# Kernel tuning notes

Measured on AMD Instinct MI355X. Metric: run time of the kernel, lower is better.

Reference implementation:

```python
import jax, jax.numpy as jnp
import numpy as np

T = 4096          # num tokens
HID = 2048        # hidden_size
HQ = 32           # num q heads
HKV = 8           # num kv heads
G = HQ // HKV     # GQA group size
D = 128           # head_dim (q/k)
DV = 96           # v_head_dim
W = 512           # sliding window (= query block size)
THETA = 1e6
Q_SIZE, K_SIZE, V_SIZE = HQ * D, HKV * D, HKV * DV


def setup_inputs() -> dict:
    key = jax.random.key(0)
    k1, k2, k3, k4 = jax.random.split(key, 4)
    positions = jnp.arange(T, dtype=jnp.int32)
    hidden_states = jax.random.normal(k1, (T, HID), dtype=jnp.float32)
    qkv_w = jax.random.normal(k2, (Q_SIZE + K_SIZE + V_SIZE, HID), dtype=jnp.float32) * (HID ** -0.5)
    o_w = jax.random.normal(k3, (HID, HQ * DV), dtype=jnp.float32) * ((HQ * DV) ** -0.5)
    sink_bias = jax.random.normal(k4, (HQ,), dtype=jnp.float32)
    return {"positions": positions, "hidden_states": hidden_states,
            "qkv_w": qkv_w, "o_w": o_w, "sink_bias": sink_bias}


def _rope(x, positions):
    # neox-style rotate-half RoPE on full head_dim (partial_rotary_factor=1.0)
    half = D // 2
    inv_freq = 1.0 / (THETA ** (jnp.arange(0, half, dtype=jnp.float32) / half))
    ang = positions.astype(jnp.float32)[:, None] * inv_freq[None, :]   # [T, D/2]
    cos = jnp.cos(ang)[:, None, :]
    sin = jnp.sin(ang)[:, None, :]
    x1, x2 = x[..., :half], x[..., half:]
    return jnp.concatenate([x1 * cos - x2 * sin, x2 * cos + x1 * sin], axis=-1)


def _swa_with_sink(q, k, v, sink_bias):
    # q: [T, HKV, G, D], k: [T, HKV, D], v: [T, HKV, DV]
    nb = T // W
    scale = D ** -0.5
    qb = q.reshape(nb, W, HKV, G, D)
    # per query block i, keys/values from global span [(i-1)*W, (i+1)*W)
    k_pad = jnp.pad(k, ((W, 0), (0, 0), (0, 0)))
    v_pad = jnp.pad(v, ((W, 0), (0, 0), (0, 0)))
    idx = jnp.arange(nb)[:, None] * W + jnp.arange(2 * W)[None, :]     # [nb, 2W]
    k_ext = k_pad[idx]                                                 # [nb, 2W, HKV, D]
    v_ext = v_pad[idx]                                                 # [nb, 2W, HKV, DV]
    # mask: rel = t - j in [0, W); exclude left-pad keys (key_pos < 0)
    r = jnp.arange(W)[:, None]
    c = jnp.arange(2 * W)[None, :]
    rel = W + r - c                                                    # [W, 2W]
    key_pos = (jnp.arange(nb)[:, None, None] - 1) * W + c[None]        # [nb, W(1), 2W]
    mask = (rel >= 0) & (rel < W) & (key_pos >= 0)                     # [nb, W, 2W]
    scores = jnp.einsum('nrkgd,nckd->nkgrc', qb, k_ext) * scale        # [nb,HKV,G,W,2W]
    scores = jnp.where(mask[:, None, None, :, :], scores, -jnp.inf)
    sink = jnp.broadcast_to(sink_bias.reshape(HKV, G)[None, :, :, None, None],
                            (nb, HKV, G, W, 1))
    logits = jnp.concatenate([scores, sink], axis=-1)                  # [...,2W+1]
    p = jax.nn.softmax(logits, axis=-1)[..., :-1]                      # drop sink column
    out = jnp.einsum('nkgrc,nckd->nrkgd', p, v_ext)                    # [nb,W,HKV,G,DV]
    return out.reshape(T, HQ * DV)


def reference(positions, hidden_states, qkv_w, o_w, sink_bias):
    qkv = hidden_states @ qkv_w.T                                      # [T, Q+K+V]
    q, k, v = jnp.split(qkv, [Q_SIZE, Q_SIZE + K_SIZE], axis=-1)
    q = q.reshape(T, HQ, D)
    k = k.reshape(T, HKV, D)
    v = v.reshape(T, HKV, DV)
    q = _rope(q, positions).reshape(T, HKV, G, D)
    k = _rope(k, positions)
    attn = _swa_with_sink(q, k, v, sink_bias)                          # [T, HQ*DV]
    return attn @ o_w.T                                                # [T, HID]
```

## Files before the change

### kernel.cpp

```cpp
#include <hip/hip_runtime.h>
#include <hip/hip_bf16.h>
#include <stdint.h>

#define T_SEQ 4096
#define HIDDEN 2048
#define NQH 32
#define NKVH 8
#define DH 128
#define DVH 96
#define WWIN 512
#define QKVN 5888
#define KOFF 4096
#define VOFF 5120
#define ATTN 3072
#define QSCALE 0.08838834764831845f

typedef uint16_t u16;
typedef uint32_t u32;
typedef __bf16 bfrag8 __attribute__((ext_vector_type(8)));
typedef float f32x4v __attribute__((ext_vector_type(4)));
typedef float f32x16 __attribute__((ext_vector_type(16)));

__device__ __forceinline__ u16 f2bf(float x) {
  u32 u = __float_as_uint(x);
  return (u16)((u + 0x7fffu + ((u >> 16) & 1u)) >> 16);
}
__device__ __forceinline__ float bf2f(u16 v) { return __uint_as_float(((u32)v) << 16); }

__device__ __forceinline__ void gload16(const u16* src, char* ldst) {
  __builtin_amdgcn_global_load_lds((const __attribute__((address_space(1))) u32*)src,
                                   (__attribute__((address_space(3))) u32*)ldst, 16, 0, 0);
}

__global__ void cvt_kernel(const float* __restrict__ in, u16* __restrict__ out, int n4) {
  int i = blockIdx.x * blockDim.x + threadIdx.x;
  int st = gridDim.x * blockDim.x;
  for (; i < n4; i += st) {
    float4 v = ((const float4*)in)[i];
    ushort4 o;
    o.x = f2bf(v.x); o.y = f2bf(v.y); o.z = f2bf(v.z); o.w = f2bf(v.w);
    ((ushort4*)out)[i] = o;
  }
}

template<int OUT_F32>
__global__ __launch_bounds__(512, 2) void gemm_v3(const u16* __restrict__ A,
                                                  const u16* __restrict__ B,
                                                  void* __restrict__ Cp,
                                                  int M, int N, int K, int nbm) {
  extern __shared__ char lds[];
  const int tid = threadIdx.x;
  const int w = tid >> 6, lane = tid & 63;
  const int wr = w >> 1, wc = w & 1;
  const int r5 = lane & 31, kg = lane >> 5;

  const int nwg = gridDim.x;
  int bid = (int)blockIdx.x;
  if ((nwg & 7) == 0) bid = (bid & 7) * (nwg >> 3) + (bid >> 3);
  const int bm = (bid % nbm) * 256;
  const int bn = (bid / nbm) * 128;
  const int NT = K >> 6;

  f32x16 acc[2][2];
#pragma unroll
  for (int mb = 0; mb < 2; mb++)
#pragma unroll
    for (int nb = 0; nb < 2; nb++)
#pragma unroll
      for (int i = 0; i < 16; i++) acc[mb][nb][i] = 0.f;

  const int q = r5 * 128 + ((kg ^ (r5 & 7)) << 4);

  auto stageA = [&](int t) {
    char* dst = lds + (t % 3) * 49152;
    const u16* Abase = A + (size_t)bm * K + ((size_t)t << 6);
#pragma unroll
    for (int i = 0; i < 4; i++) {
      int D = (w * 4 + i) * 1024 + lane * 16;
      int row = D >> 7;
      int kb = (D ^ ((row & 7) << 4)) & 127;
      gload16(Abase + (size_t)row * K + (kb >> 1), dst + D);
    }
  };
  auto stageB = [&](int t) {
    char* dst = lds + (t % 3) * 49152 + 32768;
    const u16* Bbase = B + (size_t)bn * K + ((size_t)t << 6);
#pragma unroll
    for (int i = 0; i < 2; i++) {
      int D = (w * 2 + i) * 1024 + lane * 16;
      int row = D >> 7;
      int kb = (D ^ ((row & 7) << 4)) & 127;
      gload16(Bbase + (size_t)row * K + (kb >> 1), dst + D);
    }
  };

  stageA(0); stageB(0);

  for (int t = 0; t < NT; ++t) {
    const char* Ab = lds + (t % 3) * 49152 + wr * 8192;
    const char* Bb = lds + (t % 3) * 49152 + 32768 + wc * 8192;
    if (t + 1 < NT) {
      stageA(t + 1);
      stageB(t + 1);
      asm volatile("s_waitcnt vmcnt(6)");
    } else {
      asm volatile("s_waitcnt vmcnt(0)");
    }
    asm volatile("s_barrier" ::: "memory");

    bfrag8 af[2][2], bf[2][2];
#pragma unroll
    for (int ks = 0; ks < 2; ks++) {
#pragma unroll
      for (int mb = 0; mb < 2; mb++)
        af[mb][ks] = *(const bfrag8*)(Ab + mb * 4096 + (q ^ (ks << 5)));
#pragma unroll
      for (int nb = 0; nb < 2; nb++)
        bf[nb][ks] = *(const bfrag8*)(Bb + nb * 4096 + (q ^ (ks << 5)));
    }
    __builtin_amdgcn_s_setprio(1);
#pragma unroll
    for (int ks = 0; ks < 2; ks++)
#pragma unroll
      for (int mb = 0; mb < 2; mb++)
#pragma unroll
        for (int nb = 0; nb < 2; nb++)
          acc[mb][nb] = __builtin_amdgcn_mfma_f32_32x32x16_bf16(af[mb][ks], bf[nb][ks], acc[mb][nb], 0, 0, 0);
    __builtin_amdgcn_s_setprio(0);

    bfrag8 af2[2][2], bf2[2][2];
#pragma unroll
    for (int ks = 0; ks < 2; ks++) {
#pragma unroll
      for (int mb = 0; mb < 2; mb++)
        af2[mb][ks] = *(const bfrag8*)(Ab + mb * 4096 + (q ^ ((ks + 2) << 5)));
#pragma unroll
      for (int nb = 0; nb < 2; nb++)
        bf2[nb][ks] = *(const bfrag8*)(Bb + nb * 4096 + (q ^ ((ks + 2) << 5)));
    }
    __builtin_amdgcn_s_setprio(1);
#pragma unroll
    for (int ks = 0; ks < 2; ks++)
#pragma unroll
      for (int mb = 0; mb < 2; mb++)
#pragma unroll
        for (int nb = 0; nb < 2; nb++)
          acc[mb][nb] = __builtin_amdgcn_mfma_f32_32x32x16_bf16(af2[mb][ks], bf2[nb][ks], acc[mb][nb], 0, 0, 0);
    __builtin_amdgcn_s_setprio(0);
  }

  const int rb0 = bm + wr * 64;
  const int cb0 = bn + wc * 64;
#pragma unroll
  for (int mb = 0; mb < 2; mb++)
#pragma unroll
    for (int nb = 0; nb < 2; nb++)
#pragma unroll
      for (int i = 0; i < 16; i++) {
        int rowl = (i & 3) + 8 * (i >> 2) + 4 * kg;
        size_t off = (size_t)(rb0 + mb * 32 + rowl) * N + cb0 + nb * 32 + r5;
        if (OUT_F32) ((float*)Cp)[off] = acc[mb][nb][i];
        else         ((u16*)Cp)[off] = f2bf(acc[mb][nb][i]);
      }
}

template<int OUT_F32>
__global__ __launch_bounds__(256) void gemm_nt(const u16* __restrict__ A,
                                               const u16* __restrict__ B,
                                               void* __restrict__ Cp,
                                               int M, int N, int K) {
  __shared__ u16 Asm[128 * 32];
  __shared__ u16 Bsm[128 * 32];
  const int tid = threadIdx.x;
  const int wv = tid >> 6, lane = tid & 63;
  const int bm = blockIdx.x * 128, bn = blockIdx.y * 128;
  const int wm = (wv >> 1) * 64, wn = (wv & 1) * 64;
  const int srow = lane >> 2;
  const int scol = (lane & 3) * 8;
  const int fr = lane & 15, fk = (lane >> 4) * 8;
  f32x4v acc[4][4];
#pragma unroll
  for (int i = 0; i < 4; i++)
#pragma unroll
    for (int j = 0; j < 4; j++) acc[i][j] = {0.f, 0.f, 0.f, 0.f};

  for (int kt = 0; kt < K; kt += 32) {
    __syncthreads();
#pragma unroll
    for (int c = 0; c < 2; c++) {
      const int ci = wv * 2 + c;
      const u16* ga = A + (size_t)(bm + ci * 16 + srow) * K + kt + scol;
      const u16* gb = B + (size_t)(bn + ci * 16 + srow) * K + kt + scol;
      gload16(ga, (char*)(Asm + ci * 512));
      gload16(gb, (char*)(Bsm + ci * 512));
    }
    __syncthreads();
    bfrag8 af[4], bf[4];
#pragma unroll
    for (int i = 0; i < 4; i++) af[i] = *(const bfrag8*)(Asm + (wm + i * 16 + fr) * 32 + fk);
#pragma unroll
    for (int j = 0; j < 4; j++) bf[j] = *(const bfrag8*)(Bsm + (wn + j * 16 + fr) * 32 + fk);
#pragma unroll
    for (int i = 0; i < 4; i++)
#pragma unroll
      for (int j = 0; j < 4; j++)
        acc[i][j] = __builtin_amdgcn_mfma_f32_16x16x32_bf16(af[i], bf[j], acc[i][j], 0, 0, 0);
  }
  const int orow = (lane >> 4) * 4, ocol = lane & 15;
#pragma unroll
  for (int i = 0; i < 4; i++)
#pragma unroll
    for (int j = 0; j < 4; j++) {
      size_t base = (size_t)(bm + wm + i * 16 + orow) * N + (size_t)(bn + wn + j * 16 + ocol);
#pragma unroll
      for (int r = 0; r < 4; r++) {
        if (OUT_F32) ((float*)Cp)[base + (size_t)r * N] = acc[i][j][r];
        else         ((u16*)Cp)[base + (size_t)r * N] = f2bf(acc[i][j][r]);
      }
    }
}

__global__ void rope_kernel(u16* __restrict__ qkv, const int* __restrict__ pos) {
  int gid = blockIdx.x * 256 + threadIdx.x;
  int d = gid & 63;
  int r = gid >> 6;
  int hh = r % 40;
  int t = r / 40;
  if (t >= T_SEQ) return;
  int off = (hh < 32) ? hh * 128 : KOFF + (hh - 32) * 128;
  u16* p = qkv + (size_t)t * QKVN + off + d;
  float x1 = bf2f(p[0]);
  float x2 = bf2f(p[64]);
  float inv_freq = exp2f(-(float)d * 0.3114307588956852f);
  float ang = (float)pos[t] * inv_freq;
  float c = cosf(ang), s = sinf(ang);
  float y1 = x1 * c - x2 * s;
  float y2 = x2 * c + x1 * s;
  if (hh < 32) { y1 *= QSCALE; y2 *= QSCALE; }
  p[0] = f2bf(y1);
  p[64] = f2bf(y2);
}

__global__ __launch_bounds__(256) void vt_kernel(const u16* __restrict__ qkv,
                                                 u16* __restrict__ vt) {
  __shared__ u16 tile[64][100];
  const int t0 = blockIdx.x * 64;
  const int hk = blockIdx.y;
  const int tid = threadIdx.x;
#pragma unroll
  for (int i = 0; i < 3; i++) {
    int idx = i * 256 + tid;
    int row = idx / 12, ch = idx % 12;
    const u16* g = qkv + (size_t)(t0 + row) * QKVN + VOFF + hk * DVH + ch * 8;
    uint2 a = *(const uint2*)g;
    uint2 b = *(const uint2*)(g + 4);
    *(uint2*)&tile[row][ch * 8] = a;
    *(uint2*)&tile[row][ch * 8 + 4] = b;
  }
  __syncthreads();
#pragma unroll
  for (int i = 0; i < 3; i++) {
    int idx = i * 256 + tid;
    int dv = idx >> 3, tc = (idx & 7) * 8;
    union { uint4 v4; u16 s[8]; } o;
#pragma unroll
    for (int j = 0; j < 8; j++) o.s[j] = tile[tc + j][dv];
    *(uint4*)(vt + (((size_t)(hk * 96 + dv)) << 12) + t0 + tc) = o.v4;
  }
}

__global__ __launch_bounds__(256, 2) void attn_mfma(const u16* __restrict__ qkv,
                                                    const u16* __restrict__ vt,
                                                    const float* __restrict__ sink_bias,
                                                    u16* __restrict__ attn_out) {
  extern __shared__ char smem[];

  const int tid = threadIdx.x;
  const int wv = tid >> 6;
  const int lane = tid & 63;
  const int g = lane >> 4;
  const int c = lane & 15;
  const int t0 = blockIdx.x * 32;
  const int hk = blockIdx.y;
  const int h = hk * 4 + wv;
  u16* pw = (u16*)(smem + 57344 + wv * 4096);

  bfrag8 qf[2][4];
#pragma unroll
  for (int m = 0; m < 2; m++)
#pragma unroll
    for (int kf = 0; kf < 4; kf++)
      qf[m][kf] = *(const bfrag8*)(qkv + (size_t)(t0 + m * 16 + c) * QKVN + h * DH + kf * 32 + g * 8);

  f32x4v acc_o[2][6];
#pragma unroll
  for (int m = 0; m < 2; m++)
#pragma unroll
    for (int n = 0; n < 6; n++) acc_o[m][n] = {0.f, 0.f, 0.f, 0.f};

  const float sb = sink_bias[h];
  float m_run[2][4], l_run[2][4];
#pragma unroll
  for (int m = 0; m < 2; m++)
#pragma unroll
    for (int r = 0; r < 4; r++) { m_run[m][r] = sb; l_run[m][r] = 1.0f; }

  int cb0 = t0 - (WWIN - 1);
  cb0 = (cb0 < 0) ? 0 : (cb0 & ~63);
  const int nc = (t0 + 32 - cb0 + 63) >> 6;

  auto stage = [&](int ci) {
    const int cb = cb0 + ci * 64;
    char* kd = smem + (ci & 1) * 16384;
    char* vd = smem + 32768 + (ci & 1) * 12288;
#pragma unroll
    for (int it = 0; it < 4; it++) {
      int dest = it * 4096 + tid * 16;
      int row = dest >> 8;
      int src = dest ^ ((row & 7) << 4);
      gload16(qkv + (size_t)(cb + row) * QKVN + KOFF + hk * DH + ((src & 255) >> 1), kd + dest);
    }
#pragma unroll
    for (int it = 0; it < 3; it++) {
      int dest = it * 4096 + tid * 16;
      int row = dest >> 7;
      int src = dest ^ ((row & 7) << 4);
      gload16(vt + (((size_t)(hk * 96 + row)) << 12) + cb + ((src & 127) >> 1), vd + dest);
    }
  };

  stage(0);
  if (nc > 1) stage(1);

  for (int ci = 0; ci < nc; ci++) {
    const int cb = cb0 + ci * 64;
    const char* k_lds = smem + (ci & 1) * 16384;
    const char* v_lds = smem + 32768 + (ci & 1) * 12288;
    if (ci + 1 < nc) asm volatile("s_waitcnt vmcnt(7)");
    else             asm volatile("s_waitcnt vmcnt(0)");
    asm volatile("s_barrier" ::: "memory");

    f32x4v s[2][4];
#pragma unroll
    for (int m = 0; m < 2; m++)
#pragma unroll
      for (int n = 0; n < 4; n++) s[m][n] = {0.f, 0.f, 0.f, 0.f};
#pragma unroll
    for (int kf = 0; kf < 4; kf++) {
      bfrag8 kb[4];
#pragma unroll
      for (int n = 0; n < 4; n++) {
        int key = n * 16 + c;
        int byt = ((key << 8) + (kf << 6) + (g << 4)) ^ ((key & 7) << 4);
        kb[n] = *(const bfrag8*)(k_lds + byt);
      }
#pragma unroll
      for (int m = 0; m < 2; m++)
#pragma unroll
        for (int n = 0; n < 4; n++)
          s[m][n] = __builtin_amdgcn_mfma_f32_16x16x32_bf16(qf[m][kf], kb[n], s[m][n], 0, 0, 0);
    }

    if ((cb + 63 > t0) || (cb + WWIN < t0 + 32)) {
#pragma unroll
      for (int m = 0; m < 2; m++)
#pragma unroll
        for (int n = 0; n < 4; n++)
#pragma unroll
          for (int r = 0; r < 4; r++) {
            int rel = (t0 + m * 16 + g * 4 + r) - (cb + n * 16 + c);
            if (!(rel >= 0 && rel < WWIN)) s[m][n][r] = -3.0e38f;
          }
    }

    float corr[2][4];
#pragma unroll
    for (int m = 0; m < 2; m++)
#pragma unroll
      for (int r = 0; r < 4; r++) {
        float v0 = fmaxf(fmaxf(s[m][0][r], s[m][1][r]), fmaxf(s[m][2][r], s[m][3][r]));
        v0 = fmaxf(v0, __shfl_xor(v0, 1));
        v0 = fmaxf(v0, __shfl_xor(v0, 2));
        v0 = fmaxf(v0, __shfl_xor(v0, 4));
        v0 = fmaxf(v0, __shfl_xor(v0, 8));
        float mn = fmaxf(m_run[m][r], v0);
        corr[m][r] = __expf(m_run[m][r] - mn);
        m_run[m][r] = mn;
        float p0 = __expf(s[m][0][r] - mn);
        float p1 = __expf(s[m][1][r] - mn);
        float p2 = __expf(s[m][2][r] - mn);
        float p3 = __expf(s[m][3][r] - mn);
        s[m][0][r] = p0; s[m][1][r] = p1; s[m][2][r] = p2; s[m][3][r] = p3;
        float rs = p0 + p1 + p2 + p3;
        rs += __shfl_xor(rs, 1);
        rs += __shfl_xor(rs, 2);
        rs += __shfl_xor(rs, 4);
        rs += __shfl_xor(rs, 8);
        l_run[m][r] = l_run[m][r] * corr[m][r] + rs;
      }
#pragma unroll
    for (int m = 0; m < 2; m++)
#pragma unroll
      for (int n = 0; n < 6; n++)
#pragma unroll
      for (int r = 0; r < 4; r++) acc_o[m][n][r] *= corr[m][r];

#pragma unroll
    for (int m = 0; m < 2; m++)
#pragma unroll
      for (int n = 0; n < 4; n++) {
        u32 lo = (u32)f2bf(s[m][n][0]) | ((u32)f2bf(s[m][n][1]) << 16);
        u32 hi = (u32)f2bf(s[m][n][2]) | ((u32)f2bf(s[m][n][3]) << 16);
        int byt = ((m * 2 + (n >> 1)) << 10) | (g << 3) | ((c & 3) << 5) |
                  (((c >> 2) & 1) << 9) | ((((n & 1) * 2) + (c >> 3)) << 7);
        uint2 u; u.x = lo; u.y = hi;
        *(uint2*)((char*)pw + byt) = u;
      }

#pragma unroll
    for (int ks = 0; ks < 2; ks++) {
      bfrag8 pa[2];
#pragma unroll
      for (int m = 0; m < 2; m++) {
        union { bfrag8 v; u16 s16[8]; } u;
#pragma unroll
        for (int j = 0; j < 4; j++) {
          int e = ((m * 2 + ks) << 9) + c + j * 16 + g * 64;
          u.s16[j] = pw[e];
          u.s16[4 + j] = pw[e + 256];
        }
        pa[m] = u.v;
      }
#pragma unroll
      for (int n = 0; n < 6; n++) {
        int dv = n * 16 + c;
        int byt = ((dv << 7) + (ks << 6) + (g << 4)) ^ ((dv & 7) << 4);
        bfrag8 vb = *(const bfrag8*)(v_lds + byt);
#pragma unroll
        for (int m = 0; m < 2; m++)
          acc_o[m][n] = __builtin_amdgcn_mfma_f32_16x16x32_bf16(pa[m], vb, acc_o[m][n], 0, 0, 0);
      }
    }

    asm volatile("s_barrier" ::: "memory");
    if (ci + 2 < nc) stage(ci + 2);
  }

#pragma unroll
  for (int m = 0; m < 2; m++) {
    float inv[4];
#pragma unroll
    for (int r = 0; r < 4; r++) inv[r] = 1.0f / l_run[m][r];
#pragma unroll
    for (int n = 0; n < 6; n++)
#pragma unroll
      for (int r = 0; r < 4; r++) {
        int tq = t0 + m * 16 + g * 4 + r;
        attn_out[(size_t)tq * ATTN + h * DVH + n * 16 + c] = f2bf(acc_o[m][n][r] * inv[r]);
      }
  }
}

extern "C" void kernel_launch(void* const* d_in, const int* in_sizes, int n_in,
                              void* d_out, int out_size, void* d_ws, size_t ws_size,
                              hipStream_t stream) {
  const int* positions = (const int*)d_in[0];
  const float* hidden = (const float*)d_in[1];
  const float* qkv_w = (const float*)d_in[2];
  const float* o_w = (const float*)d_in[3];
  const float* sink = (const float*)d_in[4];
  char* ws = (char*)d_ws;

  u16* hs_bf   = (u16*)(ws + 0);
  u16* w1_bf   = (u16*)(ws + 16777216);
  u16* attn_bf = (u16*)(ws + 0);
  u16* vt_buf  = (u16*)(ws + 25165824);
  u16* w2_bf   = (u16*)(ws + 40894464);
  u16* qkv_bf  = (u16*)(ws + 53477376);

  bool v3Ok =
    (hipFuncSetAttribute((const void*)&gemm_v3<0>,
                         hipFuncAttributeMaxDynamicSharedMemorySize, 147456) == hipSuccess) &&
    (hipFuncSetAttribute((const void*)&gemm_v3<1>,
                         hipFuncAttributeMaxDynamicSharedMemorySize, 147456) == hipSuccess);
  bool atOk = (hipFuncSetAttribute((const void*)&attn_mfma,
                 hipFuncAttributeMaxDynamicSharedMemorySize, 73728) == hipSuccess);
  (void)atOk;

  cvt_kernel<<<dim3(1024), dim3(256), 0, stream>>>(hidden, hs_bf, 8388608 / 4);
  cvt_kernel<<<dim3(1024), dim3(256), 0, stream>>>(qkv_w, w1_bf, 12058624 / 4);
  cvt_kernel<<<dim3(1024), dim3(256), 0, stream>>>(o_w, w2_bf, 6291456 / 4);

  if (v3Ok)
    gemm_v3<0><<<dim3(736), dim3(512), 147456, stream>>>(hs_bf, w1_bf, (void*)qkv_bf,
                                                         T_SEQ, QKVN, HIDDEN, 16);
  else
    gemm_nt<0><<<dim3(32, 46), dim3(256), 0, stream>>>(hs_bf, w1_bf, (void*)qkv_bf,
                                                       T_SEQ, QKVN, HIDDEN);

  rope_kernel<<<dim3(40960), dim3(256), 0, stream>>>(qkv_bf, positions);
  vt_kernel<<<dim3(T_SEQ / 64, NKVH), dim3(256), 0, stream>>>(qkv_bf, vt_buf);
  attn_mfma<<<dim3(T_SEQ / 32, NKVH), dim3(256), 73728, stream>>>(qkv_bf, vt_buf, sink, attn_bf);

  if (v3Ok)
    gemm_v3<1><<<dim3(256), dim3(512), 147456, stream>>>(attn_bf, w2_bf, d_out,
                                                         T_SEQ, HIDDEN, ATTN, 16);
  else
    gemm_nt<1><<<dim3(32, 16), dim3(256), 0, stream>>>(attn_bf, w2_bf, d_out,
                                                       T_SEQ, HIDDEN, ATTN);
}
```

Before: 313.5 us.

## Double attention query tile, vectorize RoPE, fuse fp32→bf16 conversions into one launch

The attention kernel now processes 64 queries per block instead of 32, split into two 32-row halves per KV chunk. Each staged K/V chunk is reused across twice as many queries, cutting redundant global loads and the block count. The output rescale is skipped when no running max grew, RoPE handles 8 elements per thread with 16-byte loads, and the three conversion kernels are merged into one launch. The larger query tile raises register pressure (qf, acc_o and softmax state double) and halves grid parallelism for attention.

```diff
diff --git a/kernel.cpp b/kernel.cpp
--- a/kernel.cpp
+++ b/kernel.cpp
@@ -32,14 +32,24 @@
                                    (__attribute__((address_space(3))) u32*)ldst, 16, 0, 0);
 }
 
-__global__ void cvt_kernel(const float* __restrict__ in, u16* __restrict__ out, int n4) {
+__global__ void cvt3_kernel(const float* __restrict__ i1, const float* __restrict__ i2,
+                            const float* __restrict__ i3,
+                            u16* __restrict__ o1, u16* __restrict__ o2, u16* __restrict__ o3,
+                            int n1, int n2, int n3) {
   int i = blockIdx.x * blockDim.x + threadIdx.x;
   int st = gridDim.x * blockDim.x;
-  for (; i < n4; i += st) {
-    float4 v = ((const float4*)in)[i];
+  int total = n1 + n2 + n3;
+  for (; i < total; i += st) {
+    const float4* src;
+    ushort4* dst;
+    int j;
+    if (i < n1) { src = (const float4*)i1; dst = (ushort4*)o1; j = i; }
+    else if (i < n1 + n2) { src = (const float4*)i2; dst = (ushort4*)o2; j = i - n1; }
+    else { src = (const float4*)i3; dst = (ushort4*)o3; j = i - n1 - n2; }
+    float4 v = src[j];
     ushort4 o;
     o.x = f2bf(v.x); o.y = f2bf(v.y); o.z = f2bf(v.z); o.w = f2bf(v.w);
-    ((ushort4*)out)[i] = o;
+    dst[j] = o;
   }
 }
 
@@ -222,23 +232,33 @@
 
 __global__ void rope_kernel(u16* __restrict__ qkv, const int* __restrict__ pos) {
   int gid = blockIdx.x * 256 + threadIdx.x;
-  int d = gid & 63;
-  int r = gid >> 6;
+  int dc = gid & 7;
+  int r = gid >> 3;
   int hh = r % 40;
   int t = r / 40;
   if (t >= T_SEQ) return;
   int off = (hh < 32) ? hh * 128 : KOFF + (hh - 32) * 128;
-  u16* p = qkv + (size_t)t * QKVN + off + d;
-  float x1 = bf2f(p[0]);
-  float x2 = bf2f(p[64]);
-  float inv_freq = exp2f(-(float)d * 0.3114307588956852f);
-  float ang = (float)pos[t] * inv_freq;
-  float c = cosf(ang), s = sinf(ang);
-  float y1 = x1 * c - x2 * s;
-  float y2 = x2 * c + x1 * s;
-  if (hh < 32) { y1 *= QSCALE; y2 *= QSCALE; }
-  p[0] = f2bf(y1);
-  p[64] = f2bf(y2);
+  u16* p = qkv + (size_t)t * QKVN + off + dc * 8;
+  uint4 a = *(const uint4*)p;
+  uint4 b = *(const uint4*)(p + 64);
+  const u32* aw = (const u32*)&a;
+  const u32* bw = (const u32*)&b;
+  float pt = (float)pos[t];
+  float sc = (hh < 32) ? QSCALE : 1.0f;
+  union { uint4 v; u16 s[8]; } ra, rb;
+#pragma unroll
+  for (int j = 0; j < 8; j++) {
+    int d = dc * 8 + j;
+    float inv_freq = exp2f(-(float)d * 0.3114307588956852f);
+    float ang = pt * inv_freq;
+    float cs = cosf(ang), sn = sinf(ang);
+    float x1 = bf2f((u16)(aw[j >> 1] >> ((j & 1) * 16)));
+    float x2 = bf2f((u16)(bw[j >> 1] >> ((j & 1) * 16)));
+    ra.s[j] = f2bf((x1 * cs - x2 * sn) * sc);
+    rb.s[j] = f2bf((x2 * cs + x1 * sn) * sc);
+  }
+  *(uint4*)p = ra.v;
+  *(uint4*)(p + 64) = rb.v;
 }
 
 __global__ __launch_bounds__(256) void vt_kernel(const u16* __restrict__ qkv,
@@ -280,34 +300,34 @@
   const int lane = tid & 63;
   const int g = lane >> 4;
   const int c = lane & 15;
-  const int t0 = blockIdx.x * 32;
+  const int t0 = blockIdx.x * 64;
   const int hk = blockIdx.y;
   const int h = hk * 4 + wv;
   u16* pw = (u16*)(smem + 57344 + wv * 4096);
 
-  bfrag8 qf[2][4];
-#pragma unroll
-  for (int m = 0; m < 2; m++)
+  bfrag8 qf[4][4];
+#pragma unroll
+  for (int m = 0; m < 4; m++)
 #pragma unroll
     for (int kf = 0; kf < 4; kf++)
       qf[m][kf] = *(const bfrag8*)(qkv + (size_t)(t0 + m * 16 + c) * QKVN + h * DH + kf * 32 + g * 8);
 
-  f32x4v acc_o[2][6];
-#pragma unroll
-  for (int m = 0; m < 2; m++)
+  f32x4v acc_o[4][6];
+#pragma unroll
+  for (int m = 0; m < 4; m++)
 #pragma unroll
     for (int n = 0; n < 6; n++) acc_o[m][n] = {0.f, 0.f, 0.f, 0.f};
 
   const float sb = sink_bias[h];
-  float m_run[2][4], l_run[2][4];
-#pragma unroll
-  for (int m = 0; m < 2; m++)
+  float m_run[4][4], l_run[4][4];
+#pragma unroll
+  for (int m = 0; m < 4; m++)
 #pragma unroll
     for (int r = 0; r < 4; r++) { m_run[m][r] = sb; l_run[m][r] = 1.0f; }
 
   int cb0 = t0 - (WWIN - 1);
   cb0 = (cb0 < 0) ? 0 : (cb0 & ~63);
-  const int nc = (t0 + 32 - cb0 + 63) >> 6;
+  const int nc = ((t0 - cb0) >> 6) + 1;
 
   auto stage = [&](int ci) {
     const int cb = cb0 + ci * 64;
@@ -340,105 +360,116 @@
     else             asm volatile("s_waitcnt vmcnt(0)");
     asm volatile("s_barrier" ::: "memory");
 
-    f32x4v s[2][4];
-#pragma unroll
-    for (int m = 0; m < 2; m++)
-#pragma unroll
-      for (int n = 0; n < 4; n++) s[m][n] = {0.f, 0.f, 0.f, 0.f};
-#pragma unroll
-    for (int kf = 0; kf < 4; kf++) {
-      bfrag8 kb[4];
-#pragma unroll
-      for (int n = 0; n < 4; n++) {
-        int key = n * 16 + c;
-        int byt = ((key << 8) + (kf << 6) + (g << 4)) ^ ((key & 7) << 4);
-        kb[n] = *(const bfrag8*)(k_lds + byt);
-      }
-#pragma unroll
-      for (int m = 0; m < 2; m++)
-#pragma unroll
-        for (int n = 0; n < 4; n++)
-          s[m][n] = __builtin_amdgcn_mfma_f32_16x16x32_bf16(qf[m][kf], kb[n], s[m][n], 0, 0, 0);
-    }
-
-    if ((cb + 63 > t0) || (cb + WWIN < t0 + 32)) {
-#pragma unroll
-      for (int m = 0; m < 2; m++)
-#pragma unroll
-        for (int n = 0; n < 4; n++)
-#pragma unroll
-          for (int r = 0; r < 4; r++) {
-            int rel = (t0 + m * 16 + g * 4 + r) - (cb + n * 16 + c);
-            if (!(rel >= 0 && rel < WWIN)) s[m][n][r] = -3.0e38f;
+    const bool edge = (cb + 63 > t0) || (cb + WWIN < t0 + 64);
+
+#pragma unroll
+    for (int mh = 0; mh < 2; mh++) {
+      f32x4v s[2][4];
+#pragma unroll
+      for (int ml = 0; ml < 2; ml++)
+#pragma unroll
+        for (int n = 0; n < 4; n++) s[ml][n] = {0.f, 0.f, 0.f, 0.f};
+#pragma unroll
+      for (int kf = 0; kf < 4; kf++) {
+        bfrag8 kb[4];
+#pragma unroll
+        for (int n = 0; n < 4; n++) {
+          int key = n * 16 + c;
+          int byt = ((key << 8) + (kf << 6) + (g << 4)) ^ ((key & 7) << 4);
+          kb[n] = *(const bfrag8*)(k_lds + byt);
+        }
+#pragma unroll
+        for (int ml = 0; ml < 2; ml++)
+#pragma unroll
+          for (int n = 0; n < 4; n++)
+            s[ml][n] = __builtin_amdgcn_mfma_f32_16x16x32_bf16(qf[mh * 2 + ml][kf], kb[n], s[ml][n], 0, 0, 0);
+      }
+
+      if (edge) {
+#pragma unroll
+        for (int ml = 0; ml < 2; ml++)
+#pragma unroll
+          for (int n = 0; n < 4; n++)
+#pragma unroll
+            for (int r = 0; r < 4; r++) {
+              int rel = (t0 + (mh * 2 + ml) * 16 + g * 4 + r) - (cb + n * 16 + c);
+              if (!(rel >= 0 && rel < WWIN)) s[ml][n][r] = -3.0e38f;
+            }
+      }
+
+      float corr[2][4];
+      bool grew = false;
+#pragma unroll
+      for (int ml = 0; ml < 2; ml++)
+#pragma unroll
+        for (int r = 0; r < 4; r++) {
+          const int M = mh * 2 + ml;
+          float v0 = fmaxf(fmaxf(s[ml][0][r], s[ml][1][r]), fmaxf(s[ml][2][r], s[ml][3][r]));
+          v0 = fmaxf(v0, __shfl_xor(v0, 1));
+          v0 = fmaxf(v0, __shfl_xor(v0, 2));
+          v0 = fmaxf(v0, __shfl_xor(v0, 4));
+          v0 = fmaxf(v0, __shfl_xor(v0, 8));
+          float mo = m_run[M][r];
+          float mn = fmaxf(mo, v0);
+          corr[ml][r] = __expf(mo - mn);
+          grew |= (mn > mo);
+          m_run[M][r] = mn;
+          float p0 = __expf(s[ml][0][r] - mn);
+          float p1 = __expf(s[ml][1][r] - mn);
+          float p2 = __expf(s[ml][2][r] - mn);
+          float p3 = __expf(s[ml][3][r] - mn);
+          s[ml][0][r] = p0; s[ml][1][r] = p1; s[ml][2][r] = p2; s[ml][3][r] = p3;
+          float rs = p0 + p1 + p2 + p3;
+          rs += __shfl_xor(rs, 1);
+          rs += __shfl_xor(rs, 2);
+          rs += __shfl_xor(rs, 4);
+          rs += __shfl_xor(rs, 8);
+          l_run[M][r] = l_run[M][r] * corr[ml][r] + rs;
+        }
+      if (__any(grew)) {
+#pragma unroll
+        for (int ml = 0; ml < 2; ml++)
+#pragma unroll
+          for (int n = 0; n < 6; n++)
+#pragma unroll
+            for (int r = 0; r < 4; r++) acc_o[mh * 2 + ml][n][r] *= corr[ml][r];
+      }
+
+#pragma unroll
+      for (int ml = 0; ml < 2; ml++)
+#pragma unroll
+        for (int n = 0; n < 4; n++) {
+          u32 lo = (u32)f2bf(s[ml][n][0]) | ((u32)f2bf(s[ml][n][1]) << 16);
+          u32 hi = (u32)f2bf(s[ml][n][2]) | ((u32)f2bf(s[ml][n][3]) << 16);
+          int byt = ((ml * 2 + (n >> 1)) << 10) | (g << 3) | ((c & 3) << 5) |
+                    (((c >> 2) & 1) << 9) | ((((n & 1) * 2) + (c >> 3)) << 7);
+          uint2 u; u.x = lo; u.y = hi;
+          *(uint2*)((char*)pw + byt) = u;
+        }
+
+#pragma unroll
+      for (int ks = 0; ks < 2; ks++) {
+        bfrag8 pa[2];
+#pragma unroll
+        for (int ml = 0; ml < 2; ml++) {
+          union { bfrag8 v; u16 s16[8]; } u;
+#pragma unroll
+          for (int j = 0; j < 4; j++) {
+            int e = ((ml * 2 + ks) << 9) + c + j * 16 + g * 64;
+            u.s16[j] = pw[e];
+            u.s16[4 + j] = pw[e + 256];
           }
-    }
-
-    float corr[2][4];
-#pragma unroll
-    for (int m = 0; m < 2; m++)
-#pragma unroll
-      for (int r = 0; r < 4; r++) {
-        float v0 = fmaxf(fmaxf(s[m][0][r], s[m][1][r]), fmaxf(s[m][2][r], s[m][3][r]));
-        v0 = fmaxf(v0, __shfl_xor(v0, 1));
-        v0 = fmaxf(v0, __shfl_xor(v0, 2));
-        v0 = fmaxf(v0, __shfl_xor(v0, 4));
-        v0 = fmaxf(v0, __shfl_xor(v0, 8));
-        float mn = fmaxf(m_run[m][r], v0);
-        corr[m][r] = __expf(m_run[m][r] - mn);
-        m_run[m][r] = mn;
-        float p0 = __expf(s[m][0][r] - mn);
-        float p1 = __expf(s[m][1][r] - mn);
-        float p2 = __expf(s[m][2][r] - mn);
-        float p3 = __expf(s[m][3][r] - mn);
-        s[m][0][r] = p0; s[m][1][r] = p1; s[m][2][r] = p2; s[m][3][r] = p3;
-        float rs = p0 + p1 + p2 + p3;
-        rs += __shfl_xor(rs, 1);
-        rs += __shfl_xor(rs, 2);
-        rs += __shfl_xor(rs, 4);
-        rs += __shfl_xor(rs, 8);
-        l_run[m][r] = l_run[m][r] * corr[m][r] + rs;
-      }
-#pragma unroll
-    for (int m = 0; m < 2; m++)
-#pragma unroll
-      for (int n = 0; n < 6; n++)
-#pragma unroll
-      for (int r = 0; r < 4; r++) acc_o[m][n][r] *= corr[m][r];
-
-#pragma unroll
-    for (int m = 0; m < 2; m++)
-#pragma unroll
-      for (int n = 0; n < 4; n++) {
-        u32 lo = (u32)f2bf(s[m][n][0]) | ((u32)f2bf(s[m][n][1]) << 16);
-        u32 hi = (u32)f2bf(s[m][n][2]) | ((u32)f2bf(s[m][n][3]) << 16);
-        int byt = ((m * 2 + (n >> 1)) << 10) | (g << 3) | ((c & 3) << 5) |
-                  (((c >> 2) & 1) << 9) | ((((n & 1) * 2) + (c >> 3)) << 7);
-        uint2 u; u.x = lo; u.y = hi;
-        *(uint2*)((char*)pw + byt) = u;
-      }
-
-#pragma unroll
-    for (int ks = 0; ks < 2; ks++) {
-      bfrag8 pa[2];
-#pragma unroll
-      for (int m = 0; m < 2; m++) {
-        union { bfrag8 v; u16 s16[8]; } u;
-#pragma unroll
-        for (int j = 0; j < 4; j++) {
-          int e = ((m * 2 + ks) << 9) + c + j * 16 + g * 64;
-          u.s16[j] = pw[e];
-          u.s16[4 + j] = pw[e + 256];
+          pa[ml] = u.v;
         }
-        pa[m] = u.v;
-      }
-#pragma unroll
-      for (int n = 0; n < 6; n++) {
-        int dv = n * 16 + c;
-        int byt = ((dv << 7) + (ks << 6) + (g << 4)) ^ ((dv & 7) << 4);
-        bfrag8 vb = *(const bfrag8*)(v_lds + byt);
-#pragma unroll
-        for (int m = 0; m < 2; m++)
-          acc_o[m][n] = __builtin_amdgcn_mfma_f32_16x16x32_bf16(pa[m], vb, acc_o[m][n], 0, 0, 0);
+#pragma unroll
+        for (int n = 0; n < 6; n++) {
+          int dv = n * 16 + c;
+          int byt = ((dv << 7) + (ks << 6) + (g << 4)) ^ ((dv & 7) << 4);
+          bfrag8 vb = *(const bfrag8*)(v_lds + byt);
+#pragma unroll
+          for (int ml = 0; ml < 2; ml++)
+            acc_o[mh * 2 + ml][n] = __builtin_amdgcn_mfma_f32_16x16x32_bf16(pa[ml], vb, acc_o[mh * 2 + ml][n], 0, 0, 0);
+        }
       }
     }
 
@@ -447,7 +478,7 @@
   }
 
 #pragma unroll
-  for (int m = 0; m < 2; m++) {
+  for (int m = 0; m < 4; m++) {
     float inv[4];
 #pragma unroll
     for (int r = 0; r < 4; r++) inv[r] = 1.0f / l_run[m][r];
@@ -483,13 +514,12 @@
                          hipFuncAttributeMaxDynamicSharedMemorySize, 147456) == hipSuccess) &&
     (hipFuncSetAttribute((const void*)&gemm_v3<1>,
                          hipFuncAttributeMaxDynamicSharedMemorySize, 147456) == hipSuccess);
-  bool atOk = (hipFuncSetAttribute((const void*)&attn_mfma,
-                 hipFuncAttributeMaxDynamicSharedMemorySize, 73728) == hipSuccess);
-  (void)atOk;
-
-  cvt_kernel<<<dim3(1024), dim3(256), 0, stream>>>(hidden, hs_bf, 8388608 / 4);
-  cvt_kernel<<<dim3(1024), dim3(256), 0, stream>>>(qkv_w, w1_bf, 12058624 / 4);
-  cvt_kernel<<<dim3(1024), dim3(256), 0, stream>>>(o_w, w2_bf, 6291456 / 4);
+  (void)hipFuncSetAttribute((const void*)&attn_mfma,
+                            hipFuncAttributeMaxDynamicSharedMemorySize, 73728);
+
+  cvt3_kernel<<<dim3(2048), dim3(256), 0, stream>>>(hidden, qkv_w, o_w,
+                                                    hs_bf, w1_bf, w2_bf,
+                                                    2097152, 3014656, 1572864);
 
   if (v3Ok)
     gemm_v3<0><<<dim3(736), dim3(512), 147456, stream>>>(hs_bf, w1_bf, (void*)qkv_bf,
@@ -498,9 +528,9 @@
     gemm_nt<0><<<dim3(32, 46), dim3(256), 0, stream>>>(hs_bf, w1_bf, (void*)qkv_bf,
                                                        T_SEQ, QKVN, HIDDEN);
 
-  rope_kernel<<<dim3(40960), dim3(256), 0, stream>>>(qkv_bf, positions);
+  rope_kernel<<<dim3(5120), dim3(256), 0, stream>>>(qkv_bf, positions);
   vt_kernel<<<dim3(T_SEQ / 64, NKVH), dim3(256), 0, stream>>>(qkv_bf, vt_buf);
-  attn_mfma<<<dim3(T_SEQ / 32, NKVH), dim3(256), 73728, stream>>>(qkv_bf, vt_buf, sink, attn_bf);
+  attn_mfma<<<dim3(T_SEQ / 64, NKVH), dim3(256), 73728, stream>>>(qkv_bf, vt_buf, sink, attn_bf);
 
   if (v3Ok)
     gemm_v3<1><<<dim3(256), dim3(512), 147456, stream>>>(attn_bf, w2_bf, d_out,
```

After: 385.4 us. 1.23x slower.

## Fuse weight conversions, vectorize RoPE, skip unneeded accumulator rescale

Applied to the files above, without the earlier changes.

Merges the three fp32-to-bf16 conversion launches into one kernel over the concatenated ranges, which saves launch overhead and tail effects. Changes RoPE so each thread handles 8 contiguous elements with 128-bit loads and stores instead of scalar 16-bit accesses, which also cuts the grid size by 8x. In the attention loop, the output accumulator rescale is skipped when no row's running max grew in the wave. This adds a wave vote and branch in exchange for fewer multiplies.

```diff
diff --git a/kernel.cpp b/kernel.cpp
--- a/kernel.cpp
+++ b/kernel.cpp
@@ -32,14 +32,24 @@
                                    (__attribute__((address_space(3))) u32*)ldst, 16, 0, 0);
 }
 
-__global__ void cvt_kernel(const float* __restrict__ in, u16* __restrict__ out, int n4) {
+__global__ void cvt3_kernel(const float* __restrict__ i1, const float* __restrict__ i2,
+                            const float* __restrict__ i3,
+                            u16* __restrict__ o1, u16* __restrict__ o2, u16* __restrict__ o3,
+                            int n1, int n2, int n3) {
   int i = blockIdx.x * blockDim.x + threadIdx.x;
   int st = gridDim.x * blockDim.x;
-  for (; i < n4; i += st) {
-    float4 v = ((const float4*)in)[i];
+  int total = n1 + n2 + n3;
+  for (; i < total; i += st) {
+    const float4* src;
+    ushort4* dst;
+    int j;
+    if (i < n1) { src = (const float4*)i1; dst = (ushort4*)o1; j = i; }
+    else if (i < n1 + n2) { src = (const float4*)i2; dst = (ushort4*)o2; j = i - n1; }
+    else { src = (const float4*)i3; dst = (ushort4*)o3; j = i - n1 - n2; }
+    float4 v = src[j];
     ushort4 o;
     o.x = f2bf(v.x); o.y = f2bf(v.y); o.z = f2bf(v.z); o.w = f2bf(v.w);
-    ((ushort4*)out)[i] = o;
+    dst[j] = o;
   }
 }
 
@@ -222,23 +232,33 @@
 
 __global__ void rope_kernel(u16* __restrict__ qkv, const int* __restrict__ pos) {
   int gid = blockIdx.x * 256 + threadIdx.x;
-  int d = gid & 63;
-  int r = gid >> 6;
+  int dc = gid & 7;
+  int r = gid >> 3;
   int hh = r % 40;
   int t = r / 40;
   if (t >= T_SEQ) return;
   int off = (hh < 32) ? hh * 128 : KOFF + (hh - 32) * 128;
-  u16* p = qkv + (size_t)t * QKVN + off + d;
-  float x1 = bf2f(p[0]);
-  float x2 = bf2f(p[64]);
-  float inv_freq = exp2f(-(float)d * 0.3114307588956852f);
-  float ang = (float)pos[t] * inv_freq;
-  float c = cosf(ang), s = sinf(ang);
-  float y1 = x1 * c - x2 * s;
-  float y2 = x2 * c + x1 * s;
-  if (hh < 32) { y1 *= QSCALE; y2 *= QSCALE; }
-  p[0] = f2bf(y1);
-  p[64] = f2bf(y2);
+  u16* p = qkv + (size_t)t * QKVN + off + dc * 8;
+  uint4 a = *(const uint4*)p;
+  uint4 b = *(const uint4*)(p + 64);
+  const u32* aw = (const u32*)&a;
+  const u32* bw = (const u32*)&b;
+  float pt = (float)pos[t];
+  float sc = (hh < 32) ? QSCALE : 1.0f;
+  union { uint4 v; u16 s[8]; } ra, rb;
+#pragma unroll
+  for (int j = 0; j < 8; j++) {
+    int d = dc * 8 + j;
+    float inv_freq = exp2f(-(float)d * 0.3114307588956852f);
+    float ang = pt * inv_freq;
+    float cs = cosf(ang), sn = sinf(ang);
+    float x1 = bf2f((u16)(aw[j >> 1] >> ((j & 1) * 16)));
+    float x2 = bf2f((u16)(bw[j >> 1] >> ((j & 1) * 16)));
+    ra.s[j] = f2bf((x1 * cs - x2 * sn) * sc);
+    rb.s[j] = f2bf((x2 * cs + x1 * sn) * sc);
+  }
+  *(uint4*)p = ra.v;
+  *(uint4*)(p + 64) = rb.v;
 }
 
 __global__ __launch_bounds__(256) void vt_kernel(const u16* __restrict__ qkv,
@@ -374,6 +394,7 @@
     }
 
     float corr[2][4];
+    bool grew = false;
 #pragma unroll
     for (int m = 0; m < 2; m++)
 #pragma unroll
@@ -383,8 +404,10 @@
         v0 = fmaxf(v0, __shfl_xor(v0, 2));
         v0 = fmaxf(v0, __shfl_xor(v0, 4));
         v0 = fmaxf(v0, __shfl_xor(v0, 8));
-        float mn = fmaxf(m_run[m][r], v0);
-        corr[m][r] = __expf(m_run[m][r] - mn);
+        float mo = m_run[m][r];
+        float mn = fmaxf(mo, v0);
+        corr[m][r] = __expf(mo - mn);
+        grew |= (mn > mo);
         m_run[m][r] = mn;
         float p0 = __expf(s[m][0][r] - mn);
         float p1 = __expf(s[m][1][r] - mn);
@@ -398,12 +421,14 @@
         rs += __shfl_xor(rs, 8);
         l_run[m][r] = l_run[m][r] * corr[m][r] + rs;
       }
-#pragma unroll
-    for (int m = 0; m < 2; m++)
-#pragma unroll
-      for (int n = 0; n < 6; n++)
-#pragma unroll
-      for (int r = 0; r < 4; r++) acc_o[m][n][r] *= corr[m][r];
+    if (__any(grew)) {
+#pragma unroll
+      for (int m = 0; m < 2; m++)
+#pragma unroll
+        for (int n = 0; n < 6; n++)
+#pragma unroll
+        for (int r = 0; r < 4; r++) acc_o[m][n][r] *= corr[m][r];
+    }
 
 #pragma unroll
     for (int m = 0; m < 2; m++)
@@ -483,13 +508,12 @@
                          hipFuncAttributeMaxDynamicSharedMemorySize, 147456) == hipSuccess) &&
     (hipFuncSetAttribute((const void*)&gemm_v3<1>,
                          hipFuncAttributeMaxDynamicSharedMemorySize, 147456) == hipSuccess);
-  bool atOk = (hipFuncSetAttribute((const void*)&attn_mfma,
-                 hipFuncAttributeMaxDynamicSharedMemorySize, 73728) == hipSuccess);
-  (void)atOk;
-
-  cvt_kernel<<<dim3(1024), dim3(256), 0, stream>>>(hidden, hs_bf, 8388608 / 4);
-  cvt_kernel<<<dim3(1024), dim3(256), 0, stream>>>(qkv_w, w1_bf, 12058624 / 4);
-  cvt_kernel<<<dim3(1024), dim3(256), 0, stream>>>(o_w, w2_bf, 6291456 / 4);
+  (void)hipFuncSetAttribute((const void*)&attn_mfma,
+                            hipFuncAttributeMaxDynamicSharedMemorySize, 73728);
+
+  cvt3_kernel<<<dim3(2048), dim3(256), 0, stream>>>(hidden, qkv_w, o_w,
+                                                    hs_bf, w1_bf, w2_bf,
+                                                    2097152, 3014656, 1572864);
 
   if (v3Ok)
     gemm_v3<0><<<dim3(736), dim3(512), 147456, stream>>>(hs_bf, w1_bf, (void*)qkv_bf,
@@ -498,7 +522,7 @@
     gemm_nt<0><<<dim3(32, 46), dim3(256), 0, stream>>>(hs_bf, w1_bf, (void*)qkv_bf,
                                                        T_SEQ, QKVN, HIDDEN);
 
-  rope_kernel<<<dim3(40960), dim3(256), 0, stream>>>(qkv_bf, positions);
+  rope_kernel<<<dim3(5120), dim3(256), 0, stream>>>(qkv_bf, positions);
   vt_kernel<<<dim3(T_SEQ / 64, NKVH), dim3(256), 0, stream>>>(qkv_bf, vt_buf);
   attn_mfma<<<dim3(T_SEQ / 32, NKVH), dim3(256), 73728, stream>>>(qkv_bf, vt_buf, sink, attn_bf);
 
```

New measurement: 308.7 us, median of 3. About the same (-1.5%).
